# Kernel optimization log

Hardware: AMD Instinct MI355X
Metric: run time of the kernel (lower is better)

## Reference

```python
import jax, jax.numpy as jnp
import numpy as np

N_PROT, N_SUB = 50000, 2000
D_PROT, D_SUB, D_PROJ, KERNEL, N_INT = 256, 256, 128, 16, 64


def setup_inputs() -> dict:
    key = jax.random.key(0)
    ks = jax.random.split(key, 8)
    init = lambda k, shape: jax.random.normal(k, shape, dtype=jnp.float32) * 0.02
    return {
        "prot_node": jax.random.normal(ks[0], (N_PROT, D_PROT), dtype=jnp.float32),
        "sub_node": jax.random.normal(ks[1], (N_SUB, D_SUB), dtype=jnp.float32),
        "int_index": jax.random.randint(ks[2], (N_INT,), 0, N_SUB),
        "Wp": init(ks[3], (D_PROT, D_PROJ)),  # prot_proj weight (in,out layout)
        "bp": jnp.zeros((D_PROJ,), jnp.float32),
        "Ws": init(ks[4], (D_SUB, D_PROJ)),   # sub_proj weight
        "bs": jnp.zeros((D_PROJ,), jnp.float32),
        "wa": init(ks[5], (2 * D_PROJ,)),     # attention_proj weight (out dim 1)
        "ba": jnp.zeros((), jnp.float32),
        "sub_out": init(ks[6], (D_PROJ, D_SUB)),
        "prot_out": init(ks[7], (D_PROJ, D_PROT)),
    }


def reference(prot_node, sub_node, int_index, Wp, bp, Ws, bs, wa, ba, sub_out, prot_out):
    K = KERNEL
    prot_proj = prot_node @ Wp + bp                              # [N, D]
    # reaction potion: sum of projected interacting substrate nodes -> [D]
    reaction = jnp.sum(sub_node[int_index] @ Ws + bs, axis=0)
    num_windows = prot_node.shape[0] - K + 1                     # W
    # attention_proj(concat(window_row, reaction)) splits linearly:
    #   logit = window_row . wa[:D] + reaction . wa[D:] + ba
    # The reaction part is a per-row constant -> compute per-node logits once.
    w1, w2 = wa[:D_PROJ], wa[D_PROJ:]
    g = prot_proj @ w1 + (reaction @ w2 + ba)                    # [N]
    # sliding-window gather indices [W, K]
    idx = jnp.arange(num_windows)[:, None] + jnp.arange(K)[None, :]
    attn = jax.nn.softmax(g[idx], axis=1)                        # [W, K] softmax over window
    local = jnp.einsum('wk,wkd->wd', attn, prot_proj[idx])       # [W, D]
    scores = local + reaction                                    # [W, D]
    # rank windows and pick the best
    top = jnp.argmax(jnp.sum(scores, axis=1))
    top_score = scores[top]                                      # [D]
    # scatter updates back into the node features
    # (set matches torch's non-accumulating fancy-index += for duplicate indices;
    #  the added delta is identical for every row anyway)
    sub_new = sub_node.at[int_index].set(sub_node[int_index] + top_score @ sub_out)
    prot_delta = top_score @ prot_out                            # [D_PROT]
    win = jax.lax.dynamic_slice(prot_node, (top, 0), (K, D_PROT))
    prot_new = jax.lax.dynamic_update_slice(prot_node, win + prot_delta, (top, 0))
    return prot_new, sub_new, int_index
```

## Files before the change

kernel.cpp:

```cpp
#include <hip/hip_runtime.h>
#include <hip/hip_bf16.h>
#include <math.h>

#define N_PROT 50000
#define N_SUB  2000
#define D_PROT 256
#define D_SUB  256
#define D_PROJ 128
#define KW     16
#define N_INT  64
#define NWIN   (N_PROT - KW + 1)

#define OUT_SUB (N_PROT * D_PROT)
#define OUT_IDX (OUT_SUB + N_SUB * D_SUB)

#define WS_PACK  0
#define WS_REACT 2
#define WS_U1    132
#define WS_U2    388
#define WS_G     644
#define WS_P     (WS_G + N_PROT)

__global__ __launch_bounds__(256) void k_prep(
    const float* __restrict__ sub_node, const int* __restrict__ int_index,
    const float* __restrict__ Ws, const float* __restrict__ bs,
    const float* __restrict__ Wp, const float* __restrict__ wa,
    float* __restrict__ ws) {
  const int tid = threadIdx.x;
  if (blockIdx.x == 0) {
    __shared__ int   sidx[N_INT];
    __shared__ float ssum[D_SUB];
    if (tid < N_INT) sidx[tid] = int_index[tid];
    __syncthreads();
    float acc = 0.f;
    #pragma unroll 8
    for (int i = 0; i < N_INT; ++i) acc += sub_node[sidx[i] * D_SUB + tid];
    ssum[tid] = acc;
    __syncthreads();
    if (tid < D_PROJ) {
      float r = 64.0f * bs[tid];
      #pragma unroll 8
      for (int d = 0; d < D_SUB; ++d) r = fmaf(ssum[d], Ws[d * D_PROJ + tid], r);
      ws[WS_REACT + tid] = r;
    }
    if (tid == 0) *((unsigned long long*)ws) = 0ull;
  } else {
    __shared__ float swa[D_PROJ];
    if (tid < D_PROJ) swa[tid] = wa[tid];
    __syncthreads();
    float s1 = 0.f, s2 = 0.f;
    const float4* wrow = (const float4*)&Wp[tid * D_PROJ];
    #pragma unroll 8
    for (int j4 = 0; j4 < D_PROJ / 4; ++j4) {
      float4 w = wrow[j4];
      float4 a = *(const float4*)&swa[j4 * 4];
      s1 = fmaf(w.x, a.x, fmaf(w.y, a.y, fmaf(w.z, a.z, fmaf(w.w, a.w, s1))));
      s2 += w.x + w.y + w.z + w.w;
    }
    ws[WS_U1 + tid] = s1;
    ws[WS_U2 + tid] = s2;
  }
}

#define PB 782
#define SB 8

__global__ __launch_bounds__(256) void k_rows(
    const float* __restrict__ prot, const float* __restrict__ sub_node,
    const int* __restrict__ int_index, float* __restrict__ out,
    float* __restrict__ ws) {
  const int tid = threadIdx.x, lane = tid & 63, wave = tid >> 6;
  if (blockIdx.x < PB) {
    const float4 c1 = *(const float4*)&ws[WS_U1 + lane * 4];
    const float4 c2 = *(const float4*)&ws[WS_U2 + lane * 4];
    const int rbase = blockIdx.x * 64 + wave * 16;
    if (rbase + 16 <= N_PROT) {
      #pragma unroll 4
      for (int i = 0; i < 16; ++i) {
        const int r = rbase + i;
        const float4 av = *(const float4*)&prot[r * D_PROT + lane * 4];
        *(float4*)&out[r * D_PROT + lane * 4] = av;
        float g = av.x * c1.x + av.y * c1.y + av.z * c1.z + av.w * c1.w;
        float p = av.x * c2.x + av.y * c2.y + av.z * c2.z + av.w * c2.w;
        #pragma unroll
        for (int off = 32; off > 0; off >>= 1) {
          g += __shfl_xor(g, off, 64);
          p += __shfl_xor(p, off, 64);
        }
        if (lane == 0) { ws[WS_G + r] = g; ws[WS_P + r] = p; }
      }
    } else {
      for (int i = 0; i < 16; ++i) {
        const int r = rbase + i;
        if (r >= N_PROT) break;
        const float4 av = *(const float4*)&prot[r * D_PROT + lane * 4];
        *(float4*)&out[r * D_PROT + lane * 4] = av;
        float g = av.x * c1.x + av.y * c1.y + av.z * c1.z + av.w * c1.w;
        float p = av.x * c2.x + av.y * c2.y + av.z * c2.z + av.w * c2.w;
        for (int off = 32; off > 0; off >>= 1) {
          g += __shfl_xor(g, off, 64);
          p += __shfl_xor(p, off, 64);
        }
        if (lane == 0) { ws[WS_G + r] = g; ws[WS_P + r] = p; }
      }
    }
  } else {
    const int sb = blockIdx.x - PB;
    #pragma unroll 4
    for (int i = tid; i < 16000; i += 256) {
      const int gi = sb * 16000 + i;
      *(float4*)&out[OUT_SUB + gi * 4] = *(const float4*)&sub_node[gi * 4];
    }
    if (sb == 0 && tid < N_INT) out[OUT_IDX + tid] = (float)int_index[tid];
  }
}

__global__ __launch_bounds__(256) void k_window(
    const float* __restrict__ ws, unsigned long long* __restrict__ packed) {
  __shared__ float sg[256 + KW], sp[256 + KW];
  __shared__ unsigned long long wred[4];
  const int tid = threadIdx.x;
  const int w0 = blockIdx.x * 256;
  for (int i = tid; i < 256 + KW - 1; i += 256) {
    int idx = w0 + i;
    bool ok = idx < N_PROT;
    sg[i] = ok ? ws[WS_G + idx] : -1e30f;
    sp[i] = ok ? ws[WS_P + idx] : 0.f;
  }
  __syncthreads();
  int w = w0 + tid;
  unsigned long long best = 0ull;
  if (w < NWIN) {
    float m = sg[tid];
    #pragma unroll
    for (int k = 1; k < KW; ++k) m = fmaxf(m, sg[tid + k]);
    float s = 0.f, t = 0.f;
    #pragma unroll
    for (int k = 0; k < KW; ++k) {
      float e = expf(sg[tid + k] - m);
      s += e;
      t = fmaf(e, sp[tid + k], t);
    }
    t /= s;
    unsigned int b = __float_as_uint(t);
    unsigned int u = b ^ ((b & 0x80000000u) ? 0xFFFFFFFFu : 0x80000000u);
    best = ((unsigned long long)u << 32) |
           (unsigned long long)(0xFFFFFFFFu - (unsigned)w);
  }
  #pragma unroll
  for (int off = 32; off > 0; off >>= 1) {
    unsigned long long o = __shfl_xor(best, off, 64);
    if (o > best) best = o;
  }
  if ((tid & 63) == 0) wred[tid >> 6] = best;
  __syncthreads();
  if (tid == 0) {
    unsigned long long b2 = wred[0];
    for (int i = 1; i < 4; ++i) if (wred[i] > b2) b2 = wred[i];
    atomicMax(packed, b2);
  }
}

__global__ __launch_bounds__(256) void k_final(
    const float* __restrict__ prot, const float* __restrict__ sub_node,
    const int* __restrict__ int_index, const float* __restrict__ Wp,
    const float* __restrict__ bp, const float* __restrict__ sub_out,
    const float* __restrict__ prot_out, const float* __restrict__ ws,
    float* __restrict__ out) {
  __shared__ float aprot[KW][D_PROT];
  __shared__ float proj16[KW][D_PROJ];
  __shared__ float attn[KW];
  __shared__ float ts[D_PROJ];
  __shared__ float pdelta[D_PROT], sdelta[D_SUB];
  __shared__ int   sidx[N_INT];
  const int tid = threadIdx.x;
  unsigned long long pk = *(const unsigned long long*)ws;
  const int wtop = (int)(0xFFFFFFFFu - (unsigned)(pk & 0xFFFFFFFFull));

  if (tid < N_INT) sidx[tid] = int_index[tid];
  for (int i = tid; i < KW * D_PROT; i += 256) {
    int rr = i >> 8, dd = i & 255;
    aprot[rr][dd] = prot[(wtop + rr) * D_PROT + dd];
  }
  __syncthreads();
  const int j = tid & 127, half = tid >> 7;
  float accr[8];
  #pragma unroll
  for (int rr = 0; rr < 8; ++rr) accr[rr] = bp[j];
  for (int k = 0; k < D_PROT; ++k) {
    float wv = Wp[k * D_PROJ + j];
    #pragma unroll
    for (int rr = 0; rr < 8; ++rr)
      accr[rr] = fmaf(aprot[half * 8 + rr][k], wv, accr[rr]);
  }
  #pragma unroll
  for (int rr = 0; rr < 8; ++rr) proj16[half * 8 + rr][j] = accr[rr];
  __syncthreads();
  if (tid == 0) {
    float m = ws[WS_G + wtop];
    for (int k = 1; k < KW; ++k) m = fmaxf(m, ws[WS_G + wtop + k]);
    float e[KW], s = 0.f;
    for (int k = 0; k < KW; ++k) { e[k] = expf(ws[WS_G + wtop + k] - m); s += e[k]; }
    for (int k = 0; k < KW; ++k) attn[k] = e[k] / s;
  }
  __syncthreads();
  if (tid < D_PROJ) {
    float a = ws[WS_REACT + tid];
    #pragma unroll
    for (int k = 0; k < KW; ++k) a = fmaf(attn[k], proj16[k][tid], a);
    ts[tid] = a;
  }
  __syncthreads();
  {
    float pa = 0.f, sa = 0.f;
    #pragma unroll 8
    for (int jj = 0; jj < D_PROJ; ++jj) {
      float t = ts[jj];
      pa = fmaf(t, prot_out[jj * D_PROT + tid], pa);
      sa = fmaf(t, sub_out[jj * D_SUB + tid], sa);
    }
    pdelta[tid] = pa; sdelta[tid] = sa;
  }
  __syncthreads();
  for (int i = tid; i < KW * D_PROT; i += 256) {
    int rr = i >> 8, dd = i & 255;
    out[(wtop + rr) * D_PROT + dd] = aprot[rr][dd] + pdelta[dd];
  }
  for (int i = 0; i < N_INT; ++i) {
    int idx = sidx[i];
    out[OUT_SUB + idx * D_SUB + tid] = sub_node[idx * D_SUB + tid] + sdelta[tid];
  }
}

extern "C" void kernel_launch(void* const* d_in, const int* in_sizes, int n_in,
                              void* d_out, int out_size, void* d_ws, size_t ws_size,
                              hipStream_t stream) {
  const float* prot     = (const float*)d_in[0];
  const float* sub      = (const float*)d_in[1];
  const int*   idx      = (const int*)d_in[2];
  const float* Wp       = (const float*)d_in[3];
  const float* bp       = (const float*)d_in[4];
  const float* Ws       = (const float*)d_in[5];
  const float* bs       = (const float*)d_in[6];
  const float* wa       = (const float*)d_in[7];
  const float* sub_out  = (const float*)d_in[9];
  const float* prot_out = (const float*)d_in[10];
  float* out = (float*)d_out;
  float* ws  = (float*)d_ws;

  k_prep<<<2, 256, 0, stream>>>(sub, idx, Ws, bs, Wp, wa, ws);
  k_rows<<<PB + SB, 256, 0, stream>>>(prot, sub, idx, out, ws);
  k_window<<<(NWIN + 255) / 256, 256, 0, stream>>>(ws, (unsigned long long*)ws);
  k_final<<<1, 256, 0, stream>>>(prot, sub, idx, Wp, bp, sub_out, prot_out, ws, out);
}
```

Measured before the change: 183.4 us.

## Fuse four kernels into one cooperative kernel with grid syncs

Replaces the four-kernel launch sequence with a single cooperative kernel that runs prep, row projection and copy, window scoring, and final update as phases separated by grid.sync(). Each row block now recomputes the Wp·wa and row-sum vectors into shared memory itself, so the separate prep launch and its dependency go away. The aim is to remove launch gaps and inter-kernel serialization. The trade-offs are a large shared-memory footprint per block, which may limit occupancy, and grid-wide barrier cost. The old four-kernel path is kept as a fallback if the cooperative launch fails.

New measurement: 392.3 us. 114% more time.

```diff
diff --git a/kernel.cpp b/kernel.cpp
--- a/kernel.cpp
+++ b/kernel.cpp
@@ -1,6 +1,8 @@
 #include <hip/hip_runtime.h>
-#include <hip/hip_bf16.h>
+#include <hip/hip_cooperative_groups.h>
 #include <math.h>
+
+namespace cg = cooperative_groups;
 
 #define N_PROT 50000
 #define N_SUB  2000
@@ -21,59 +23,52 @@
 #define WS_G     644
 #define WS_P     (WS_G + N_PROT)
 
-__global__ __launch_bounds__(256) void k_prep(
-    const float* __restrict__ sub_node, const int* __restrict__ int_index,
-    const float* __restrict__ Ws, const float* __restrict__ bs,
-    const float* __restrict__ Wp, const float* __restrict__ wa,
-    float* __restrict__ ws) {
-  const int tid = threadIdx.x;
-  if (blockIdx.x == 0) {
-    __shared__ int   sidx[N_INT];
-    __shared__ float ssum[D_SUB];
-    if (tid < N_INT) sidx[tid] = int_index[tid];
-    __syncthreads();
-    float acc = 0.f;
-    #pragma unroll 8
-    for (int i = 0; i < N_INT; ++i) acc += sub_node[sidx[i] * D_SUB + tid];
-    ssum[tid] = acc;
-    __syncthreads();
-    if (tid < D_PROJ) {
-      float r = 64.0f * bs[tid];
-      #pragma unroll 8
-      for (int d = 0; d < D_SUB; ++d) r = fmaf(ssum[d], Ws[d * D_PROJ + tid], r);
-      ws[WS_REACT + tid] = r;
-    }
-    if (tid == 0) *((unsigned long long*)ws) = 0ull;
-  } else {
-    __shared__ float swa[D_PROJ];
-    if (tid < D_PROJ) swa[tid] = wa[tid];
-    __syncthreads();
-    float s1 = 0.f, s2 = 0.f;
-    const float4* wrow = (const float4*)&Wp[tid * D_PROJ];
-    #pragma unroll 8
-    for (int j4 = 0; j4 < D_PROJ / 4; ++j4) {
-      float4 w = wrow[j4];
-      float4 a = *(const float4*)&swa[j4 * 4];
-      s1 = fmaf(w.x, a.x, fmaf(w.y, a.y, fmaf(w.z, a.z, fmaf(w.w, a.w, s1))));
-      s2 += w.x + w.y + w.z + w.w;
-    }
-    ws[WS_U1 + tid] = s1;
-    ws[WS_U2 + tid] = s2;
-  }
-}
-
 #define PB 782
 #define SB 8
-
-__global__ __launch_bounds__(256) void k_rows(
+#define NBLK (PB + SB + 1)
+#define WBLK ((NWIN + 255) / 256)
+
+__global__ __launch_bounds__(256, 4) void k_all(
     const float* __restrict__ prot, const float* __restrict__ sub_node,
-    const int* __restrict__ int_index, float* __restrict__ out,
-    float* __restrict__ ws) {
+    const int* __restrict__ int_index, const float* __restrict__ Wp,
+    const float* __restrict__ bp, const float* __restrict__ Ws,
+    const float* __restrict__ bs, const float* __restrict__ wa,
+    const float* __restrict__ sub_out, const float* __restrict__ prot_out,
+    float* __restrict__ out, float* __restrict__ ws) {
+  cg::grid_group grid = cg::this_grid();
   const int tid = threadIdx.x, lane = tid & 63, wave = tid >> 6;
-  if (blockIdx.x < PB) {
-    const float4 c1 = *(const float4*)&ws[WS_U1 + lane * 4];
-    const float4 c2 = *(const float4*)&ws[WS_U2 + lane * 4];
-    const int rbase = blockIdx.x * 64 + wave * 16;
+  const int b = blockIdx.x;
+
+  __shared__ float su1[D_PROT], su2[D_PROT];
+  __shared__ float swa[D_PROJ];
+  __shared__ float sg[256 + KW], sp[256 + KW];
+  __shared__ unsigned long long wred[4];
+  __shared__ float aprot[KW][D_PROT];
+  __shared__ float proj16[KW][D_PROJ];
+  __shared__ float attn[KW];
+  __shared__ float ts[D_PROJ];
+  __shared__ float pdelta[D_PROT], sdelta[D_SUB];
+  __shared__ int   sidx[N_INT];
+
+  if (b < PB) {
+    if (tid < D_PROJ) swa[tid] = wa[tid];
+    __syncthreads();
+    {
+      float s1 = 0.f, s2 = 0.f;
+      const float4* wrow = (const float4*)&Wp[tid * D_PROJ];
+      #pragma unroll 8
+      for (int j4 = 0; j4 < D_PROJ / 4; ++j4) {
+        float4 w = wrow[j4];
+        float4 a = *(const float4*)&swa[j4 * 4];
+        s1 = fmaf(w.x, a.x, fmaf(w.y, a.y, fmaf(w.z, a.z, fmaf(w.w, a.w, s1))));
+        s2 += w.x + w.y + w.z + w.w;
+      }
+      su1[tid] = s1; su2[tid] = s2;
+    }
+    __syncthreads();
+    const float4 c1 = *(const float4*)&su1[lane * 4];
+    const float4 c2 = *(const float4*)&su2[lane * 4];
+    const int rbase = b * 64 + wave * 16;
     if (rbase + 16 <= N_PROT) {
       #pragma unroll 4
       for (int i = 0; i < 16; ++i) {
@@ -104,9 +99,203 @@
         if (lane == 0) { ws[WS_G + r] = g; ws[WS_P + r] = p; }
       }
     }
+  } else if (b < PB + SB) {
+    const int sb = b - PB;
+    #pragma unroll 4
+    for (int i = tid; i < 16000; i += 256) {
+      const int gi = sb * 16000 + i;
+      *(float4*)&out[OUT_SUB + gi * 4] = *(const float4*)&sub_node[gi * 4];
+    }
+    if (sb == 0 && tid < N_INT) out[OUT_IDX + tid] = (float)int_index[tid];
+  } else {
+    __shared__ int   ridx[N_INT];
+    __shared__ float ssum[D_SUB];
+    if (tid < N_INT) ridx[tid] = int_index[tid];
+    __syncthreads();
+    float acc = 0.f;
+    #pragma unroll 8
+    for (int i = 0; i < N_INT; ++i) acc += sub_node[ridx[i] * D_SUB + tid];
+    ssum[tid] = acc;
+    __syncthreads();
+    if (tid < D_PROJ) {
+      float r = 64.0f * bs[tid];
+      #pragma unroll 8
+      for (int d = 0; d < D_SUB; ++d) r = fmaf(ssum[d], Ws[d * D_PROJ + tid], r);
+      ws[WS_REACT + tid] = r;
+    }
+    if (tid == 0) *((unsigned long long*)ws) = 0ull;
+  }
+
+  grid.sync();
+
+  if (b < WBLK) {
+    const int w0 = b * 256;
+    for (int i = tid; i < 256 + KW - 1; i += 256) {
+      int idx = w0 + i;
+      bool ok = idx < N_PROT;
+      sg[i] = ok ? ws[WS_G + idx] : -1e30f;
+      sp[i] = ok ? ws[WS_P + idx] : 0.f;
+    }
+    __syncthreads();
+    int w = w0 + tid;
+    unsigned long long best = 0ull;
+    if (w < NWIN) {
+      float m = sg[tid];
+      #pragma unroll
+      for (int k = 1; k < KW; ++k) m = fmaxf(m, sg[tid + k]);
+      float s = 0.f, t = 0.f;
+      #pragma unroll
+      for (int k = 0; k < KW; ++k) {
+        float e = expf(sg[tid + k] - m);
+        s += e;
+        t = fmaf(e, sp[tid + k], t);
+      }
+      t /= s;
+      unsigned int bb = __float_as_uint(t);
+      unsigned int u = bb ^ ((bb & 0x80000000u) ? 0xFFFFFFFFu : 0x80000000u);
+      best = ((unsigned long long)u << 32) |
+             (unsigned long long)(0xFFFFFFFFu - (unsigned)w);
+    }
+    #pragma unroll
+    for (int off = 32; off > 0; off >>= 1) {
+      unsigned long long o = __shfl_xor(best, off, 64);
+      if (o > best) best = o;
+    }
+    if ((tid & 63) == 0) wred[tid >> 6] = best;
+    __syncthreads();
+    if (tid == 0) {
+      unsigned long long b2 = wred[0];
+      for (int i = 1; i < 4; ++i) if (wred[i] > b2) b2 = wred[i];
+      atomicMax((unsigned long long*)ws, b2);
+    }
+  }
+
+  grid.sync();
+
+  if (b == 0) {
+    unsigned long long pk = *(const unsigned long long*)ws;
+    const int wtop = (int)(0xFFFFFFFFu - (unsigned)(pk & 0xFFFFFFFFull));
+    if (tid < N_INT) sidx[tid] = int_index[tid];
+    for (int i = tid; i < KW * D_PROT; i += 256) {
+      int rr = i >> 8, dd = i & 255;
+      aprot[rr][dd] = prot[(wtop + rr) * D_PROT + dd];
+    }
+    __syncthreads();
+    const int j = tid & 127, half = tid >> 7;
+    float accr[8];
+    #pragma unroll
+    for (int rr = 0; rr < 8; ++rr) accr[rr] = bp[j];
+    for (int k = 0; k < D_PROT; ++k) {
+      float wv = Wp[k * D_PROJ + j];
+      #pragma unroll
+      for (int rr = 0; rr < 8; ++rr)
+        accr[rr] = fmaf(aprot[half * 8 + rr][k], wv, accr[rr]);
+    }
+    #pragma unroll
+    for (int rr = 0; rr < 8; ++rr) proj16[half * 8 + rr][j] = accr[rr];
+    __syncthreads();
+    if (tid == 0) {
+      float m = ws[WS_G + wtop];
+      for (int k = 1; k < KW; ++k) m = fmaxf(m, ws[WS_G + wtop + k]);
+      float e[KW], s = 0.f;
+      for (int k = 0; k < KW; ++k) { e[k] = expf(ws[WS_G + wtop + k] - m); s += e[k]; }
+      for (int k = 0; k < KW; ++k) attn[k] = e[k] / s;
+    }
+    __syncthreads();
+    if (tid < D_PROJ) {
+      float a = ws[WS_REACT + tid];
+      #pragma unroll
+      for (int k = 0; k < KW; ++k) a = fmaf(attn[k], proj16[k][tid], a);
+      ts[tid] = a;
+    }
+    __syncthreads();
+    {
+      float pa = 0.f, sa = 0.f;
+      #pragma unroll 8
+      for (int jj = 0; jj < D_PROJ; ++jj) {
+        float t = ts[jj];
+        pa = fmaf(t, prot_out[jj * D_PROT + tid], pa);
+        sa = fmaf(t, sub_out[jj * D_SUB + tid], sa);
+      }
+      pdelta[tid] = pa; sdelta[tid] = sa;
+    }
+    __syncthreads();
+    for (int i = tid; i < KW * D_PROT; i += 256) {
+      int rr = i >> 8, dd = i & 255;
+      out[(wtop + rr) * D_PROT + dd] = aprot[rr][dd] + pdelta[dd];
+    }
+    for (int i = 0; i < N_INT; ++i) {
+      int idx = sidx[i];
+      out[OUT_SUB + idx * D_SUB + tid] = sub_node[idx * D_SUB + tid] + sdelta[tid];
+    }
+  }
+}
+
+__global__ __launch_bounds__(256) void k_prep(
+    const float* __restrict__ sub_node, const int* __restrict__ int_index,
+    const float* __restrict__ Ws, const float* __restrict__ bs,
+    const float* __restrict__ Wp, const float* __restrict__ wa,
+    float* __restrict__ ws) {
+  const int tid = threadIdx.x;
+  if (blockIdx.x == 0) {
+    __shared__ int   sidx[N_INT];
+    __shared__ float ssum[D_SUB];
+    if (tid < N_INT) sidx[tid] = int_index[tid];
+    __syncthreads();
+    float acc = 0.f;
+    #pragma unroll 8
+    for (int i = 0; i < N_INT; ++i) acc += sub_node[sidx[i] * D_SUB + tid];
+    ssum[tid] = acc;
+    __syncthreads();
+    if (tid < D_PROJ) {
+      float r = 64.0f * bs[tid];
+      #pragma unroll 8
+      for (int d = 0; d < D_SUB; ++d) r = fmaf(ssum[d], Ws[d * D_PROJ + tid], r);
+      ws[WS_REACT + tid] = r;
+    }
+    if (tid == 0) *((unsigned long long*)ws) = 0ull;
+  } else {
+    __shared__ float swa[D_PROJ];
+    if (tid < D_PROJ) swa[tid] = wa[tid];
+    __syncthreads();
+    float s1 = 0.f, s2 = 0.f;
+    const float4* wrow = (const float4*)&Wp[tid * D_PROJ];
+    #pragma unroll 8
+    for (int j4 = 0; j4 < D_PROJ / 4; ++j4) {
+      float4 w = wrow[j4];
+      float4 a = *(const float4*)&swa[j4 * 4];
+      s1 = fmaf(w.x, a.x, fmaf(w.y, a.y, fmaf(w.z, a.z, fmaf(w.w, a.w, s1))));
+      s2 += w.x + w.y + w.z + w.w;
+    }
+    ws[WS_U1 + tid] = s1;
+    ws[WS_U2 + tid] = s2;
+  }
+}
+
+__global__ __launch_bounds__(256) void k_rows(
+    const float* __restrict__ prot, const float* __restrict__ sub_node,
+    const int* __restrict__ int_index, float* __restrict__ out,
+    float* __restrict__ ws) {
+  const int tid = threadIdx.x, lane = tid & 63, wave = tid >> 6;
+  if (blockIdx.x < PB) {
+    const float4 c1 = *(const float4*)&ws[WS_U1 + lane * 4];
+    const float4 c2 = *(const float4*)&ws[WS_U2 + lane * 4];
+    const int rbase = blockIdx.x * 64 + wave * 16;
+    for (int i = 0; i < 16; ++i) {
+      const int r = rbase + i;
+      if (r >= N_PROT) break;
+      const float4 av = *(const float4*)&prot[r * D_PROT + lane * 4];
+      *(float4*)&out[r * D_PROT + lane * 4] = av;
+      float g = av.x * c1.x + av.y * c1.y + av.z * c1.z + av.w * c1.w;
+      float p = av.x * c2.x + av.y * c2.y + av.z * c2.z + av.w * c2.w;
+      for (int off = 32; off > 0; off >>= 1) {
+        g += __shfl_xor(g, off, 64);
+        p += __shfl_xor(p, off, 64);
+      }
+      if (lane == 0) { ws[WS_G + r] = g; ws[WS_P + r] = p; }
+    }
   } else {
     const int sb = blockIdx.x - PB;
-    #pragma unroll 4
     for (int i = tid; i < 16000; i += 256) {
       const int gi = sb * 16000 + i;
       *(float4*)&out[OUT_SUB + gi * 4] = *(const float4*)&sub_node[gi * 4];
@@ -142,8 +331,8 @@
       t = fmaf(e, sp[tid + k], t);
     }
     t /= s;
-    unsigned int b = __float_as_uint(t);
-    unsigned int u = b ^ ((b & 0x80000000u) ? 0xFFFFFFFFu : 0x80000000u);
+    unsigned int bb = __float_as_uint(t);
+    unsigned int u = bb ^ ((bb & 0x80000000u) ? 0xFFFFFFFFu : 0x80000000u);
     best = ((unsigned long long)u << 32) |
            (unsigned long long)(0xFFFFFFFFu - (unsigned)w);
   }
@@ -176,7 +365,6 @@
   const int tid = threadIdx.x;
   unsigned long long pk = *(const unsigned long long*)ws;
   const int wtop = (int)(0xFFFFFFFFu - (unsigned)(pk & 0xFFFFFFFFull));
-
   if (tid < N_INT) sidx[tid] = int_index[tid];
   for (int i = tid; i < KW * D_PROT; i += 256) {
     int rr = i >> 8, dd = i & 255;
@@ -248,8 +436,15 @@
   float* out = (float*)d_out;
   float* ws  = (float*)d_ws;
 
-  k_prep<<<2, 256, 0, stream>>>(sub, idx, Ws, bs, Wp, wa, ws);
-  k_rows<<<PB + SB, 256, 0, stream>>>(prot, sub, idx, out, ws);
-  k_window<<<(NWIN + 255) / 256, 256, 0, stream>>>(ws, (unsigned long long*)ws);
-  k_final<<<1, 256, 0, stream>>>(prot, sub, idx, Wp, bp, sub_out, prot_out, ws, out);
-}
+  void* args[] = {(void*)&prot, (void*)&sub, (void*)&idx, (void*)&Wp,
+                  (void*)&bp,   (void*)&Ws,  (void*)&bs,  (void*)&wa,
+                  (void*)&sub_out, (void*)&prot_out, (void*)&out, (void*)&ws};
+  hipError_t e = hipLaunchCooperativeKernel((const void*)k_all, dim3(NBLK),
+                                            dim3(256), args, 0, stream);
+  if (e != hipSuccess) {
+    k_prep<<<2, 256, 0, stream>>>(sub, idx, Ws, bs, Wp, wa, ws);
+    k_rows<<<PB + SB, 256, 0, stream>>>(prot, sub, idx, out, ws);
+    k_window<<<WBLK, 256, 0, stream>>>(ws, (unsigned long long*)ws);
+    k_final<<<1, 256, 0, stream>>>(prot, sub, idx, Wp, bp, sub_out, prot_out, ws, out);
+  }
+}
```

## Fuse four kernel launches into two using last-block-done finalization

Applied to the files above, without the earlier changes.

Merges the prep kernel into the row-streaming kernel: every row block recomputes the Wp·wa and Wp row-sum vectors in shared memory, and one extra block computes the reaction vector and resets the counters. The window-softmax kernel and the single-block final kernel become one launch, where the last block to arrive (tracked by an atomic ticket after a threadfence) does the final update. This removes two launches and their inter-kernel gaps. The cost is redundant Wp reads in every row block and a dependence on atomics and memory fences for correctness.

After: 187.4 us. +2.1%, slower.

```diff
diff --git a/kernel.cpp b/kernel.cpp
--- a/kernel.cpp
+++ b/kernel.cpp
@@ -1,5 +1,4 @@
 #include <hip/hip_runtime.h>
-#include <hip/hip_bf16.h>
 #include <math.h>
 
 #define N_PROT 50000
@@ -16,64 +15,44 @@
 
 #define WS_PACK  0
 #define WS_REACT 2
-#define WS_U1    132
-#define WS_U2    388
+#define WS_CNT   130
 #define WS_G     644
 #define WS_P     (WS_G + N_PROT)
 
-__global__ __launch_bounds__(256) void k_prep(
-    const float* __restrict__ sub_node, const int* __restrict__ int_index,
+#define PB 782
+#define SB 8
+#define NBLK (PB + SB + 1)
+#define WBLK ((NWIN + 255) / 256)
+
+__global__ __launch_bounds__(256) void k_main(
+    const float* __restrict__ prot, const float* __restrict__ sub_node,
+    const int* __restrict__ int_index, const float* __restrict__ Wp,
     const float* __restrict__ Ws, const float* __restrict__ bs,
-    const float* __restrict__ Wp, const float* __restrict__ wa,
+    const float* __restrict__ wa, float* __restrict__ out,
     float* __restrict__ ws) {
-  const int tid = threadIdx.x;
-  if (blockIdx.x == 0) {
-    __shared__ int   sidx[N_INT];
-    __shared__ float ssum[D_SUB];
-    if (tid < N_INT) sidx[tid] = int_index[tid];
-    __syncthreads();
-    float acc = 0.f;
-    #pragma unroll 8
-    for (int i = 0; i < N_INT; ++i) acc += sub_node[sidx[i] * D_SUB + tid];
-    ssum[tid] = acc;
-    __syncthreads();
-    if (tid < D_PROJ) {
-      float r = 64.0f * bs[tid];
-      #pragma unroll 8
-      for (int d = 0; d < D_SUB; ++d) r = fmaf(ssum[d], Ws[d * D_PROJ + tid], r);
-      ws[WS_REACT + tid] = r;
-    }
-    if (tid == 0) *((unsigned long long*)ws) = 0ull;
-  } else {
+  const int tid = threadIdx.x, lane = tid & 63, wave = tid >> 6;
+  const int b = blockIdx.x;
+  if (b < PB) {
+    __shared__ float su1[D_PROT], su2[D_PROT];
     __shared__ float swa[D_PROJ];
     if (tid < D_PROJ) swa[tid] = wa[tid];
     __syncthreads();
-    float s1 = 0.f, s2 = 0.f;
-    const float4* wrow = (const float4*)&Wp[tid * D_PROJ];
-    #pragma unroll 8
-    for (int j4 = 0; j4 < D_PROJ / 4; ++j4) {
-      float4 w = wrow[j4];
-      float4 a = *(const float4*)&swa[j4 * 4];
-      s1 = fmaf(w.x, a.x, fmaf(w.y, a.y, fmaf(w.z, a.z, fmaf(w.w, a.w, s1))));
-      s2 += w.x + w.y + w.z + w.w;
-    }
-    ws[WS_U1 + tid] = s1;
-    ws[WS_U2 + tid] = s2;
-  }
-}
-
-#define PB 782
-#define SB 8
-
-__global__ __launch_bounds__(256) void k_rows(
-    const float* __restrict__ prot, const float* __restrict__ sub_node,
-    const int* __restrict__ int_index, float* __restrict__ out,
-    float* __restrict__ ws) {
-  const int tid = threadIdx.x, lane = tid & 63, wave = tid >> 6;
-  if (blockIdx.x < PB) {
-    const float4 c1 = *(const float4*)&ws[WS_U1 + lane * 4];
-    const float4 c2 = *(const float4*)&ws[WS_U2 + lane * 4];
-    const int rbase = blockIdx.x * 64 + wave * 16;
+    {
+      float s1 = 0.f, s2 = 0.f;
+      const float4* wrow = (const float4*)&Wp[tid * D_PROJ];
+      #pragma unroll 8
+      for (int j4 = 0; j4 < D_PROJ / 4; ++j4) {
+        float4 w = wrow[j4];
+        float4 a = *(const float4*)&swa[j4 * 4];
+        s1 = fmaf(w.x, a.x, fmaf(w.y, a.y, fmaf(w.z, a.z, fmaf(w.w, a.w, s1))));
+        s2 += w.x + w.y + w.z + w.w;
+      }
+      su1[tid] = s1; su2[tid] = s2;
+    }
+    __syncthreads();
+    const float4 c1 = *(const float4*)&su1[lane * 4];
+    const float4 c2 = *(const float4*)&su2[lane * 4];
+    const int rbase = b * 64 + wave * 16;
     if (rbase + 16 <= N_PROT) {
       #pragma unroll 4
       for (int i = 0; i < 16; ++i) {
@@ -104,21 +83,46 @@
         if (lane == 0) { ws[WS_G + r] = g; ws[WS_P + r] = p; }
       }
     }
-  } else {
-    const int sb = blockIdx.x - PB;
+  } else if (b < PB + SB) {
+    const int sb = b - PB;
     #pragma unroll 4
     for (int i = tid; i < 16000; i += 256) {
       const int gi = sb * 16000 + i;
       *(float4*)&out[OUT_SUB + gi * 4] = *(const float4*)&sub_node[gi * 4];
     }
     if (sb == 0 && tid < N_INT) out[OUT_IDX + tid] = (float)int_index[tid];
+  } else {
+    __shared__ int   ridx[N_INT];
+    __shared__ float ssum[D_SUB];
+    if (tid < N_INT) ridx[tid] = int_index[tid];
+    __syncthreads();
+    float acc = 0.f;
+    #pragma unroll 8
+    for (int i = 0; i < N_INT; ++i) acc += sub_node[ridx[i] * D_SUB + tid];
+    ssum[tid] = acc;
+    __syncthreads();
+    if (tid < D_PROJ) {
+      float r = 64.0f * bs[tid];
+      #pragma unroll 8
+      for (int d = 0; d < D_SUB; ++d) r = fmaf(ssum[d], Ws[d * D_PROJ + tid], r);
+      ws[WS_REACT + tid] = r;
+    }
+    if (tid == 0) {
+      *((unsigned long long*)ws) = 0ull;
+      ((unsigned int*)ws)[WS_CNT] = 0u;
+    }
   }
 }
 
-__global__ __launch_bounds__(256) void k_window(
-    const float* __restrict__ ws, unsigned long long* __restrict__ packed) {
+__global__ __launch_bounds__(256) void k_finish(
+    const float* __restrict__ prot, const float* __restrict__ sub_node,
+    const int* __restrict__ int_index, const float* __restrict__ Wp,
+    const float* __restrict__ bp, const float* __restrict__ sub_out,
+    const float* __restrict__ prot_out, float* __restrict__ ws,
+    float* __restrict__ out) {
   __shared__ float sg[256 + KW], sp[256 + KW];
   __shared__ unsigned long long wred[4];
+  __shared__ int slast;
   const int tid = threadIdx.x;
   const int w0 = blockIdx.x * 256;
   for (int i = tid; i < 256 + KW - 1; i += 256) {
@@ -128,55 +132,58 @@
     sp[i] = ok ? ws[WS_P + idx] : 0.f;
   }
   __syncthreads();
-  int w = w0 + tid;
-  unsigned long long best = 0ull;
-  if (w < NWIN) {
-    float m = sg[tid];
+  {
+    int w = w0 + tid;
+    unsigned long long best = 0ull;
+    if (w < NWIN) {
+      float m = sg[tid];
+      #pragma unroll
+      for (int k = 1; k < KW; ++k) m = fmaxf(m, sg[tid + k]);
+      float s = 0.f, t = 0.f;
+      #pragma unroll
+      for (int k = 0; k < KW; ++k) {
+        float e = expf(sg[tid + k] - m);
+        s += e;
+        t = fmaf(e, sp[tid + k], t);
+      }
+      t /= s;
+      unsigned int bb = __float_as_uint(t);
+      unsigned int u = bb ^ ((bb & 0x80000000u) ? 0xFFFFFFFFu : 0x80000000u);
+      best = ((unsigned long long)u << 32) |
+             (unsigned long long)(0xFFFFFFFFu - (unsigned)w);
+    }
     #pragma unroll
-    for (int k = 1; k < KW; ++k) m = fmaxf(m, sg[tid + k]);
-    float s = 0.f, t = 0.f;
-    #pragma unroll
-    for (int k = 0; k < KW; ++k) {
-      float e = expf(sg[tid + k] - m);
-      s += e;
-      t = fmaf(e, sp[tid + k], t);
-    }
-    t /= s;
-    unsigned int b = __float_as_uint(t);
-    unsigned int u = b ^ ((b & 0x80000000u) ? 0xFFFFFFFFu : 0x80000000u);
-    best = ((unsigned long long)u << 32) |
-           (unsigned long long)(0xFFFFFFFFu - (unsigned)w);
-  }
-  #pragma unroll
-  for (int off = 32; off > 0; off >>= 1) {
-    unsigned long long o = __shfl_xor(best, off, 64);
-    if (o > best) best = o;
-  }
-  if ((tid & 63) == 0) wred[tid >> 6] = best;
+    for (int off = 32; off > 0; off >>= 1) {
+      unsigned long long o = __shfl_xor(best, off, 64);
+      if (o > best) best = o;
+    }
+    if ((tid & 63) == 0) wred[tid >> 6] = best;
+  }
   __syncthreads();
   if (tid == 0) {
     unsigned long long b2 = wred[0];
     for (int i = 1; i < 4; ++i) if (wred[i] > b2) b2 = wred[i];
-    atomicMax(packed, b2);
-  }
-}
-
-__global__ __launch_bounds__(256) void k_final(
-    const float* __restrict__ prot, const float* __restrict__ sub_node,
-    const int* __restrict__ int_index, const float* __restrict__ Wp,
-    const float* __restrict__ bp, const float* __restrict__ sub_out,
-    const float* __restrict__ prot_out, const float* __restrict__ ws,
-    float* __restrict__ out) {
+    atomicMax((unsigned long long*)ws, b2);
+    __threadfence();
+    unsigned int ticket = atomicAdd(&((unsigned int*)ws)[WS_CNT], 1u);
+    slast = (ticket == WBLK - 1) ? 1 : 0;
+  }
+  __syncthreads();
+  if (!slast) return;
+
   __shared__ float aprot[KW][D_PROT];
   __shared__ float proj16[KW][D_PROJ];
   __shared__ float attn[KW];
   __shared__ float ts[D_PROJ];
   __shared__ float pdelta[D_PROT], sdelta[D_SUB];
   __shared__ int   sidx[N_INT];
-  const int tid = threadIdx.x;
-  unsigned long long pk = *(const unsigned long long*)ws;
-  const int wtop = (int)(0xFFFFFFFFu - (unsigned)(pk & 0xFFFFFFFFull));
-
+  __shared__ int   swtop;
+  if (tid == 0) {
+    unsigned long long pk = atomicMax((unsigned long long*)ws, 0ull);
+    swtop = (int)(0xFFFFFFFFu - (unsigned)(pk & 0xFFFFFFFFull));
+  }
+  __syncthreads();
+  const int wtop = swtop;
   if (tid < N_INT) sidx[tid] = int_index[tid];
   for (int i = tid; i < KW * D_PROT; i += 256) {
     int rr = i >> 8, dd = i & 255;
@@ -248,8 +255,7 @@
   float* out = (float*)d_out;
   float* ws  = (float*)d_ws;
 
-  k_prep<<<2, 256, 0, stream>>>(sub, idx, Ws, bs, Wp, wa, ws);
-  k_rows<<<PB + SB, 256, 0, stream>>>(prot, sub, idx, out, ws);
-  k_window<<<(NWIN + 255) / 256, 256, 0, stream>>>(ws, (unsigned long long*)ws);
-  k_final<<<1, 256, 0, stream>>>(prot, sub, idx, Wp, bp, sub_out, prot_out, ws, out);
+  k_main<<<NBLK, 256, 0, stream>>>(prot, sub, idx, Wp, Ws, bs, wa, out, ws);
+  k_finish<<<WBLK, 256, 0, stream>>>(prot, sub, idx, Wp, bp, sub_out, prot_out,
+                                     ws, out);
 }
```
